# Kernel tuning notes

Measured on AMD Instinct MI355X. Metric: run time of the kernel, lower is better.

## Reference

```python
import jax, jax.numpy as jnp
import numpy as np

COMMITMENT_COST = 0.25


def setup_inputs() -> dict:
    key = jax.random.key(0)
    k1, k2 = jax.random.split(key)
    N, K, D = 65536, 8192, 64
    z_e = jax.random.normal(k1, (N, D), dtype=jnp.float32)
    # xavier_uniform for Embedding(K, D): limit = sqrt(6/(K+D))
    limit = float(np.sqrt(6.0 / (K + D)))
    codebook = jax.random.uniform(k2, (K, D), dtype=jnp.float32, minval=-limit, maxval=limit)
    return {"z_e": z_e, "codebook": codebook}


def reference(z_e, codebook):
    # Squared Euclidean distances; argmin over d^2 == argmin over cdist(p=2)
    x2 = jnp.sum(z_e * z_e, axis=-1, keepdims=True)            # [N,1]
    e2 = jnp.sum(codebook * codebook, axis=-1)                 # [K]
    d2 = x2 - 2.0 * (z_e @ codebook.T) + e2                    # [N,K]
    encoding_indices = jnp.argmin(d2, axis=-1)                 # [N] int

    z_q = codebook[encoding_indices]                           # [N,D] gather

    sg = jax.lax.stop_gradient
    codebook_loss = jnp.mean((z_q - sg(z_e)) ** 2)
    commitment_loss = jnp.mean((z_e - sg(z_q)) ** 2)
    vq_loss = codebook_loss + COMMITMENT_COST * commitment_loss

    # straight-through estimator
    z_q_st = z_e + sg(z_q - z_e)
    return z_q_st, vq_loss, encoding_indices
```

## Files before the change

### kernel.cpp

```cpp
#include <hip/hip_runtime.h>
#include <hip/hip_bf16.h>

#define N_PTS 65536
#define K_CB  8192
#define D_DIM 64
#define CAPS  63

typedef float f32x4 __attribute__((ext_vector_type(4)));
typedef short s16x8 __attribute__((ext_vector_type(8)));

typedef __attribute__((address_space(1))) const unsigned int gu32;
typedef __attribute__((address_space(3))) unsigned int lu32;

__device__ __forceinline__ unsigned bfpack2(float a, float b) {
    union { __hip_bfloat162 h2; unsigned u; } cv;
    cv.h2 = __float22bfloat162_rn(make_float2(a, b));
    return cv.u;
}

__device__ __forceinline__ void gl2lds16(const void* g, void* lds) {
    __builtin_amdgcn_global_load_lds((gu32*)g, (lu32*)lds, 16, 0, 0);
}

template <int CTRL>
__device__ __forceinline__ float dpp_fmax(float v) {
    int s = __builtin_amdgcn_update_dpp(0, __float_as_int(v), CTRL, 0xf, 0xf, true);
    return fmaxf(v, __int_as_float(s));
}

__global__ __launch_bounds__(256) void vq_pack(
        const float* __restrict__ cb, unsigned short* __restrict__ cbswz) {
    int g = blockIdx.x * 256 + threadIdx.x;
    int row = g >> 3, s = g & 7;
    int u = (s ^ (row & 7)) * 8;
    const float4* p = (const float4*)(cb + (size_t)row * D_DIM + u);
    float4 a = p[0], b = p[1];
    uint4 pk;
    pk.x = bfpack2(a.x, a.y); pk.y = bfpack2(a.z, a.w);
    pk.z = bfpack2(b.x, b.y); pk.w = bfpack2(b.z, b.w);
    *(uint4*)(cbswz + (size_t)row * 64 + s * 8) = pk;
}

__global__ __launch_bounds__(256) void vq_prep(
        const float* __restrict__ z, const float* __restrict__ cb,
        float* __restrict__ e2, float* __restrict__ e2n,
        float* __restrict__ x2, float* __restrict__ bmax) {
#pragma clang fp contract(off)
    __shared__ float sm[4];
    int b = blockIdx.x;
    int lane = threadIdx.x & 63;
    int wv = threadIdx.x >> 6;
    const float* src; float* dst; int row0; bool iscb;
    if (b < 128) { src = cb; dst = e2; row0 = b * 64 + wv * 16; iscb = true; }
    else         { src = z;  dst = x2; row0 = (b - 128) * 64 + wv * 16; iscb = false; }
    float lmax = 0.f;
    for (int r = 0; r < 16; ++r) {
        int row = row0 + r;
        float v = src[(size_t)row * D_DIM + lane];
        float w = v * v;
        float ra = w;
#pragma unroll
        for (int i = 1; i < 8; ++i) ra = ra + __shfl(w, lane + 8 * i, 64);
        float r0 = __shfl(ra, 0, 64), r1 = __shfl(ra, 1, 64),
              r2 = __shfl(ra, 2, 64), r3 = __shfl(ra, 3, 64),
              r4 = __shfl(ra, 4, 64), r5 = __shfl(ra, 5, 64),
              r6 = __shfl(ra, 6, 64), r7 = __shfl(ra, 7, 64);
        if (lane == 0) {
            float s = ((r0 + r1) + (r2 + r3)) + ((r4 + r5) + (r6 + r7));
            dst[row] = s;
            if (iscb) e2n[row] = -0.5f * s;
            lmax = fmaxf(lmax, s);
        }
    }
    if (b < 128) {
        if (lane == 0) sm[wv] = lmax;
        __syncthreads();
        if (threadIdx.x == 0)
            bmax[b] = fmaxf(fmaxf(sm[0], sm[1]), fmaxf(sm[2], sm[3]));
    }
}

__device__ __forceinline__ void stage_chunk(
        const unsigned short* __restrict__ cbswz, const float* __restrict__ e2n,
        unsigned short* bufb, float* e2hb, int kc, int w, int l) {
    const char* gbase = (const char*)(cbswz + (size_t)kc * 256 * 64);
#pragma unroll
    for (int j = 0; j < 4; ++j) {
        int off = j * 8192 + w * 1024;
        gl2lds16(gbase + off + l * 16, (char*)bufb + off);
    }
    if (w == 0)
        gl2lds16(e2n + kc * 256 + l * 4, e2hb);
}

__global__ __launch_bounds__(512, 4) void vq_coarse(
        const float* __restrict__ z, const unsigned short* __restrict__ cbswz,
        const float* __restrict__ e2n, const float* __restrict__ x2,
        const float* __restrict__ bmax, int* __restrict__ cand) {
    __shared__ __align__(16) unsigned short pool[4][128 * 64];
    __shared__ __align__(16) float e2h[2][256];
    __shared__ int cntS[128];
    const int tid = threadIdx.x;
    const int w = tid >> 6, l = tid & 63, tx = l & 15, q = l >> 4;
    const int n0 = blockIdx.x * 128;

    if (tid < 128) cntS[tid] = 0;

#pragma unroll
    for (int i = 0; i < 2; ++i) {
        int lin = tid + 512 * i;
        int row = lin >> 3, u = lin & 7;
        const float4* p = (const float4*)(z + (size_t)(n0 + row) * D_DIM + u * 8);
        float4 a = p[0], b2 = p[1];
        uint4 pk;
        pk.x = bfpack2(a.x, a.y);   pk.y = bfpack2(a.z, a.w);
        pk.z = bfpack2(b2.x, b2.y); pk.w = bfpack2(b2.z, b2.w);
        *(uint4*)&pool[0][row * 64 + ((u ^ (row & 7)) * 8)] = pk;
    }

    float e2m;
    {
        float v = fmaxf(bmax[l], bmax[l + 64]);
#pragma unroll
        for (int m = 1; m < 64; m <<= 1) v = fmaxf(v, __shfl_xor(v, m, 64));
        e2m = v;
    }

    float halfW[4], A[4], M[4];
#pragma unroll
    for (int i = 0; i < 4; ++i) {
        int row = n0 + w * 16 + q * 4 + i;
        halfW[i] = 0.0175f * sqrtf(x2[row] * e2m) + 1e-4f;
        A[i] = 3.0e38f;
        M[i] = -3.4e38f;
    }
    float Amin = 3.0e38f;

    __syncthreads();
    s16x8 afr[2];
#pragma unroll
    for (int ks = 0; ks < 2; ++ks) {
        int row = w * 16 + tx;
        afr[ks] = *(const s16x8*)&pool[0][row * 64 + (((ks * 4 + q) ^ (tx & 7)) * 8)];
    }
    __syncthreads();

    stage_chunk(cbswz, e2n, &pool[0][0], e2h[0], 0, w, l);
    __syncthreads();

    for (int it = 0; it < 33; ++it) {
        const int kc = (it < 32) ? it : 0;
        const int cur = it & 1;
        if (it < 32)
            stage_chunk(cbswz, e2n, &pool[((it + 1) & 1) * 2][0], e2h[(it + 1) & 1],
                        (it + 1 < 32) ? it + 1 : 0, w, l);

        const unsigned short* cbb = &pool[cur * 2][0];
        const float* e2c = e2h[cur];
#pragma unroll
        for (int ct = 0; ct < 16; ++ct) {
            int crow = ct * 16 + tx;
            float bias = e2c[crow];
            s16x8 b0 = *(const s16x8*)&cbb[crow * 64 + ((q ^ (tx & 7)) * 8)];
            s16x8 b1 = *(const s16x8*)&cbb[crow * 64 + (((4 + q) ^ (tx & 7)) * 8)];
            f32x4 acc = {bias, bias, bias, bias};
            acc = __builtin_amdgcn_mfma_f32_16x16x32_bf16(afr[0], b0, acc, 0, 0, 0);
            acc = __builtin_amdgcn_mfma_f32_16x16x32_bf16(afr[1], b1, acc, 0, 0, 0);
            M[0] = fmaxf(M[0], acc[0]);
            M[1] = fmaxf(M[1], acc[1]);
            M[2] = fmaxf(M[2], acc[2]);
            M[3] = fmaxf(M[3], acc[3]);
            float amax = fmaxf(fmaxf(fmaxf(acc[0], acc[1]), acc[2]), acc[3]);
            if (amax >= Amin) {
                int kglob = kc * 256 + crow;
#pragma unroll
                for (int r = 0; r < 4; ++r) {
                    if (acc[r] >= A[r]) {
                        int row = w * 16 + q * 4 + r;
                        int slot = atomicAdd(&cntS[row], 1);
                        if (slot < CAPS)
                            cand[(size_t)(n0 + row) * 64 + slot] = kglob;
                    }
                }
            }
        }
        if (it < 32 && ((it == 0) || (it & 1))) {
#pragma unroll
            for (int i = 0; i < 4; ++i) {
                float v = M[i];
                v = dpp_fmax<0xB1>(v);
                v = dpp_fmax<0x4E>(v);
                v = dpp_fmax<0x124>(v);
                v = dpp_fmax<0x128>(v);
                M[i] = v;
                A[i] = v - halfW[i];
            }
            Amin = fminf(fminf(A[0], A[1]), fminf(A[2], A[3]));
        }
        __syncthreads();
    }
    if (tid < 128) cand[(size_t)(n0 + tid) * 64 + 63] = cntS[tid];
}

__device__ __forceinline__ float exact_score(const float* zr, const float* __restrict__ cb,
                                             const float* __restrict__ e2, float x2v, int k) {
    const float4* c4 = (const float4*)(cb + (size_t)k * D_DIM);
    float g = 0.f;
#pragma unroll
    for (int j = 0; j < 16; ++j) {
        float4 v = c4[j];
        g = fmaf(zr[4 * j + 0], v.x, g);
        g = fmaf(zr[4 * j + 1], v.y, g);
        g = fmaf(zr[4 * j + 2], v.z, g);
        g = fmaf(zr[4 * j + 3], v.w, g);
    }
    return fmaf(-2.f, g, x2v) + e2[k];
}

__global__ __launch_bounds__(1024, 4) void vq_rescore(
        const float* __restrict__ z, const float* __restrict__ cb,
        const float* __restrict__ e2, const float* __restrict__ x2,
        int* __restrict__ slots, float* __restrict__ idx_out,
        float* __restrict__ partials) {
    int tid = threadIdx.x;
    int r = tid >> 2, sub = tid & 3;
    int n = blockIdx.x * 256 + r;
    float zr[64];
    const float4* z4 = (const float4*)(z + (size_t)n * D_DIM);
#pragma unroll
    for (int i = 0; i < 16; ++i) {
        float4 v = z4[i];
        zr[4 * i] = v.x; zr[4 * i + 1] = v.y; zr[4 * i + 2] = v.z; zr[4 * i + 3] = v.w;
    }
    float x2v = x2[n];
    int cnt = slots[(size_t)n * 64 + 63];
    float bs = 3.4e38f; int bk = 0x7fffffff;
    if (cnt <= CAPS) {
        for (int i = sub; i < cnt; i += 4) {
            int k = slots[(size_t)n * 64 + i];
            float s = exact_score(zr, cb, e2, x2v, k);
            if (s < bs || (s == bs && k < bk)) { bs = s; bk = k; }
        }
    }
    unsigned long long mask = __ballot(cnt > CAPS && sub == 0);
    while (mask) {
        int src = __ffsll((long long)mask) - 1;
        mask &= (mask - 1);
        int rown = __shfl(n, src, 64);
        float x2s = __shfl(x2v, src, 64);
        float zs[64];
        const float4* zz = (const float4*)(z + (size_t)rown * D_DIM);
#pragma unroll
        for (int i = 0; i < 16; ++i) {
            float4 v = zz[i];
            zs[4 * i] = v.x; zs[4 * i + 1] = v.y; zs[4 * i + 2] = v.z; zs[4 * i + 3] = v.w;
        }
        float fb = 3.4e38f; int fk = 0x7fffffff;
        for (int k = (tid & 63); k < K_CB; k += 64) {
            float s = exact_score(zs, cb, e2, x2s, k);
            if (s < fb || (s == fb && k < fk)) { fb = s; fk = k; }
        }
#pragma unroll
        for (int m = 1; m < 64; m <<= 1) {
            float ov = __shfl_xor(fb, m, 64);
            int   ok = __shfl_xor(fk, m, 64);
            if (ov < fb || (ov == fb && ok < fk)) { fb = ov; fk = ok; }
        }
        if ((tid & 63) == src) { bs = fb; bk = fk; }
    }
#pragma unroll
    for (int m = 1; m < 4; m <<= 1) {
        float ov = __shfl_xor(bs, m, 64);
        int   ok = __shfl_xor(bk, m, 64);
        if (ov < bs || (ov == bs && ok < bk)) { bs = ov; bk = ok; }
    }
    __threadfence_block();

    __shared__ float red[256];
    if (sub == 0) {
        idx_out[n] = (float)bk;
        float lsum = 0.f;
        const float4* c4 = (const float4*)(cb + (size_t)bk * D_DIM);
        float4* o4 = (float4*)((float*)slots + (size_t)n * 64);
#pragma unroll
        for (int j = 0; j < 16; ++j) {
            float4 c = c4[j];
            float4 o;
            float d0 = c.x - zr[4 * j];     o.x = zr[4 * j]     + d0;
            float d1 = c.y - zr[4 * j + 1]; o.y = zr[4 * j + 1] + d1;
            float d2 = c.z - zr[4 * j + 2]; o.z = zr[4 * j + 2] + d2;
            float d3 = c.w - zr[4 * j + 3]; o.w = zr[4 * j + 3] + d3;
            lsum += d0 * d0 + d1 * d1 + d2 * d2 + d3 * d3;
            o4[j] = o;
        }
        red[r] = lsum;
    }
    __syncthreads();
    for (int s = 128; s > 0; s >>= 1) {
        if (tid < s) red[tid] += red[tid + s];
        __syncthreads();
    }
    if (tid == 0) partials[blockIdx.x] = red[0];
}

__global__ void vq_final(const float* __restrict__ partials, float* __restrict__ loss_out) {
    __shared__ float red[256];
    int tid = threadIdx.x;
    red[tid] = partials[tid];
    __syncthreads();
    for (int s = 128; s > 0; s >>= 1) {
        if (tid < s) red[tid] += red[tid + s];
        __syncthreads();
    }
    if (tid == 0) *loss_out = 1.25f * red[0] / (float)(N_PTS * D_DIM);
}

extern "C" void kernel_launch(void* const* d_in, const int* in_sizes, int n_in,
                              void* d_out, int out_size, void* d_ws, size_t ws_size,
                              hipStream_t stream) {
    const float* z  = (const float*)d_in[0];
    const float* cb = (const float*)d_in[1];
    float* out      = (float*)d_out;
    float* zq_out   = out;
    float* loss_out = out + (size_t)N_PTS * D_DIM;
    float* idx_out  = loss_out + 1;

    float* wsf = (float*)d_ws;
    float* partials = wsf;
    float* e2  = wsf + 256;
    float* e2n = wsf + 256 + K_CB;
    float* x2  = wsf + 256 + 2 * K_CB;
    unsigned short* cbswz = (unsigned short*)(wsf + 256 + 2 * K_CB + N_PTS);

    int* cand = (int*)zq_out;
    float* bmax = idx_out;

    vq_pack   <<<K_CB * 8 / 256, 256, 0, stream>>>(cb, cbswz);
    vq_prep   <<<128 + N_PTS / 64, 256, 0, stream>>>(z, cb, e2, e2n, x2, bmax);
    vq_coarse <<<N_PTS / 128, 512, 0, stream>>>(z, cbswz, e2n, x2, bmax, cand);
    vq_rescore<<<N_PTS / 256, 1024, 0, stream>>>(z, cb, e2, x2, cand, idx_out, partials);
    vq_final  <<<1, 256, 0, stream>>>(partials, loss_out);
}
```

Before: 326.8 us.

## Give each coarse wave two row tiles and split codebook columns across wave pairs

In the coarse kernel, each wave now computes two 16-row tiles against half of each 256-entry codebook chunk, so every B fragment loaded from LDS feeds two MFMA chains. A pair of waves merges row maxima through a small shared buffer after each chunk, and thresholds are now refreshed every chunk instead of every other chunk. The rescore kernel drops from four threads per row to two and uses a smaller block. The intent is to cut LDS reads per MFMA and tighten pruning, at the cost of more registers, an extra LDS exchange each iteration, and less parallelism during rescoring.

```diff
diff --git a/kernel.cpp b/kernel.cpp
--- a/kernel.cpp
+++ b/kernel.cpp
@@ -99,9 +99,11 @@
         const float* __restrict__ bmax, int* __restrict__ cand) {
     __shared__ __align__(16) unsigned short pool[4][128 * 64];
     __shared__ __align__(16) float e2h[2][256];
+    __shared__ __align__(16) float mrg[2][2][4][4][8];
     __shared__ int cntS[128];
     const int tid = threadIdx.x;
     const int w = tid >> 6, l = tid & 63, tx = l & 15, q = l >> 4;
+    const int pr = w >> 1, half = w & 1;
     const int n0 = blockIdx.x * 128;
 
     if (tid < 128) cntS[tid] = 0;
@@ -126,10 +128,10 @@
         e2m = v;
     }
 
-    float halfW[4], A[4], M[4];
-#pragma unroll
-    for (int i = 0; i < 4; ++i) {
-        int row = n0 + w * 16 + q * 4 + i;
+    float halfW[8], A[8], M[8];
+#pragma unroll
+    for (int i = 0; i < 8; ++i) {
+        int row = n0 + pr * 32 + (i >> 2) * 16 + q * 4 + (i & 3);
         halfW[i] = 0.0175f * sqrtf(x2[row] * e2m) + 1e-4f;
         A[i] = 3.0e38f;
         M[i] = -3.4e38f;
@@ -137,12 +139,14 @@
     float Amin = 3.0e38f;
 
     __syncthreads();
-    s16x8 afr[2];
-#pragma unroll
-    for (int ks = 0; ks < 2; ++ks) {
-        int row = w * 16 + tx;
-        afr[ks] = *(const s16x8*)&pool[0][row * 64 + (((ks * 4 + q) ^ (tx & 7)) * 8)];
-    }
+    s16x8 afr[2][2];
+#pragma unroll
+    for (int rt = 0; rt < 2; ++rt)
+#pragma unroll
+        for (int ks = 0; ks < 2; ++ks) {
+            int row = pr * 32 + rt * 16 + tx;
+            afr[rt][ks] = *(const s16x8*)&pool[0][row * 64 + (((ks * 4 + q) ^ (tx & 7)) * 8)];
+        }
     __syncthreads();
 
     stage_chunk(cbswz, e2n, &pool[0][0], e2h[0], 0, w, l);
@@ -158,25 +162,44 @@
         const unsigned short* cbb = &pool[cur * 2][0];
         const float* e2c = e2h[cur];
 #pragma unroll
-        for (int ct = 0; ct < 16; ++ct) {
+        for (int c8 = 0; c8 < 8; ++c8) {
+            int ct = half * 8 + c8;
             int crow = ct * 16 + tx;
             float bias = e2c[crow];
             s16x8 b0 = *(const s16x8*)&cbb[crow * 64 + ((q ^ (tx & 7)) * 8)];
             s16x8 b1 = *(const s16x8*)&cbb[crow * 64 + (((4 + q) ^ (tx & 7)) * 8)];
-            f32x4 acc = {bias, bias, bias, bias};
-            acc = __builtin_amdgcn_mfma_f32_16x16x32_bf16(afr[0], b0, acc, 0, 0, 0);
-            acc = __builtin_amdgcn_mfma_f32_16x16x32_bf16(afr[1], b1, acc, 0, 0, 0);
-            M[0] = fmaxf(M[0], acc[0]);
-            M[1] = fmaxf(M[1], acc[1]);
-            M[2] = fmaxf(M[2], acc[2]);
-            M[3] = fmaxf(M[3], acc[3]);
-            float amax = fmaxf(fmaxf(fmaxf(acc[0], acc[1]), acc[2]), acc[3]);
+            f32x4 acc0 = {bias, bias, bias, bias};
+            acc0 = __builtin_amdgcn_mfma_f32_16x16x32_bf16(afr[0][0], b0, acc0, 0, 0, 0);
+            acc0 = __builtin_amdgcn_mfma_f32_16x16x32_bf16(afr[0][1], b1, acc0, 0, 0, 0);
+            f32x4 acc1 = {bias, bias, bias, bias};
+            acc1 = __builtin_amdgcn_mfma_f32_16x16x32_bf16(afr[1][0], b0, acc1, 0, 0, 0);
+            acc1 = __builtin_amdgcn_mfma_f32_16x16x32_bf16(afr[1][1], b1, acc1, 0, 0, 0);
+            M[0] = fmaxf(M[0], acc0[0]);
+            M[1] = fmaxf(M[1], acc0[1]);
+            M[2] = fmaxf(M[2], acc0[2]);
+            M[3] = fmaxf(M[3], acc0[3]);
+            M[4] = fmaxf(M[4], acc1[0]);
+            M[5] = fmaxf(M[5], acc1[1]);
+            M[6] = fmaxf(M[6], acc1[2]);
+            M[7] = fmaxf(M[7], acc1[3]);
+            float amax = fmaxf(
+                fmaxf(fmaxf(acc0[0], acc0[1]), fmaxf(acc0[2], acc0[3])),
+                fmaxf(fmaxf(acc1[0], acc1[1]), fmaxf(acc1[2], acc1[3])));
             if (amax >= Amin) {
                 int kglob = kc * 256 + crow;
 #pragma unroll
                 for (int r = 0; r < 4; ++r) {
-                    if (acc[r] >= A[r]) {
-                        int row = w * 16 + q * 4 + r;
+                    if (acc0[r] >= A[r]) {
+                        int row = pr * 32 + q * 4 + r;
+                        int slot = atomicAdd(&cntS[row], 1);
+                        if (slot < CAPS)
+                            cand[(size_t)(n0 + row) * 64 + slot] = kglob;
+                    }
+                }
+#pragma unroll
+                for (int r = 0; r < 4; ++r) {
+                    if (acc1[r] >= A[4 + r]) {
+                        int row = pr * 32 + 16 + q * 4 + r;
                         int slot = atomicAdd(&cntS[row], 1);
                         if (slot < CAPS)
                             cand[(size_t)(n0 + row) * 64 + slot] = kglob;
@@ -184,20 +207,34 @@
                 }
             }
         }
-        if (it < 32 && ((it == 0) || (it & 1))) {
-#pragma unroll
-            for (int i = 0; i < 4; ++i) {
+        if (it < 32) {
+#pragma unroll
+            for (int i = 0; i < 8; ++i) {
                 float v = M[i];
                 v = dpp_fmax<0xB1>(v);
                 v = dpp_fmax<0x4E>(v);
                 v = dpp_fmax<0x124>(v);
                 v = dpp_fmax<0x128>(v);
                 M[i] = v;
-                A[i] = v - halfW[i];
             }
-            Amin = fminf(fminf(A[0], A[1]), fminf(A[2], A[3]));
+            if (tx == 0) {
+                *(float4*)&mrg[it & 1][half][pr][q][0] = make_float4(M[0], M[1], M[2], M[3]);
+                *(float4*)&mrg[it & 1][half][pr][q][4] = make_float4(M[4], M[5], M[6], M[7]);
+            }
         }
         __syncthreads();
+        if (it < 32) {
+            float4 oa = *(const float4*)&mrg[it & 1][half ^ 1][pr][q][0];
+            float4 ob = *(const float4*)&mrg[it & 1][half ^ 1][pr][q][4];
+            M[0] = fmaxf(M[0], oa.x); M[1] = fmaxf(M[1], oa.y);
+            M[2] = fmaxf(M[2], oa.z); M[3] = fmaxf(M[3], oa.w);
+            M[4] = fmaxf(M[4], ob.x); M[5] = fmaxf(M[5], ob.y);
+            M[6] = fmaxf(M[6], ob.z); M[7] = fmaxf(M[7], ob.w);
+#pragma unroll
+            for (int i = 0; i < 8; ++i) A[i] = M[i] - halfW[i];
+            Amin = fminf(fminf(fminf(A[0], A[1]), fminf(A[2], A[3])),
+                         fminf(fminf(A[4], A[5]), fminf(A[6], A[7])));
+        }
     }
     if (tid < 128) cand[(size_t)(n0 + tid) * 64 + 63] = cntS[tid];
 }
@@ -217,13 +254,13 @@
     return fmaf(-2.f, g, x2v) + e2[k];
 }
 
-__global__ __launch_bounds__(1024, 4) void vq_rescore(
+__global__ __launch_bounds__(512, 2) void vq_rescore(
         const float* __restrict__ z, const float* __restrict__ cb,
         const float* __restrict__ e2, const float* __restrict__ x2,
         int* __restrict__ slots, float* __restrict__ idx_out,
         float* __restrict__ partials) {
     int tid = threadIdx.x;
-    int r = tid >> 2, sub = tid & 3;
+    int r = tid >> 1, half = tid & 1;
     int n = blockIdx.x * 256 + r;
     float zr[64];
     const float4* z4 = (const float4*)(z + (size_t)n * D_DIM);
@@ -236,13 +273,13 @@
     int cnt = slots[(size_t)n * 64 + 63];
     float bs = 3.4e38f; int bk = 0x7fffffff;
     if (cnt <= CAPS) {
-        for (int i = sub; i < cnt; i += 4) {
+        for (int i = half; i < cnt; i += 2) {
             int k = slots[(size_t)n * 64 + i];
             float s = exact_score(zr, cb, e2, x2v, k);
             if (s < bs || (s == bs && k < bk)) { bs = s; bk = k; }
         }
     }
-    unsigned long long mask = __ballot(cnt > CAPS && sub == 0);
+    unsigned long long mask = __ballot(cnt > CAPS && half == 0);
     while (mask) {
         int src = __ffsll((long long)mask) - 1;
         mask &= (mask - 1);
@@ -268,16 +305,15 @@
         }
         if ((tid & 63) == src) { bs = fb; bk = fk; }
     }
-#pragma unroll
-    for (int m = 1; m < 4; m <<= 1) {
-        float ov = __shfl_xor(bs, m, 64);
-        int   ok = __shfl_xor(bk, m, 64);
+    {
+        float ov = __shfl_xor(bs, 1, 64);
+        int   ok = __shfl_xor(bk, 1, 64);
         if (ov < bs || (ov == bs && ok < bk)) { bs = ov; bk = ok; }
     }
     __threadfence_block();
 
     __shared__ float red[256];
-    if (sub == 0) {
+    if (half == 0) {
         idx_out[n] = (float)bk;
         float lsum = 0.f;
         const float4* c4 = (const float4*)(cb + (size_t)bk * D_DIM);
@@ -338,6 +374,6 @@
     vq_pack   <<<K_CB * 8 / 256, 256, 0, stream>>>(cb, cbswz);
     vq_prep   <<<128 + N_PTS / 64, 256, 0, stream>>>(z, cb, e2, e2n, x2, bmax);
     vq_coarse <<<N_PTS / 128, 512, 0, stream>>>(z, cbswz, e2n, x2, bmax, cand);
-    vq_rescore<<<N_PTS / 256, 1024, 0, stream>>>(z, cb, e2, x2, cand, idx_out, partials);
+    vq_rescore<<<N_PTS / 256, 512, 0, stream>>>(z, cb, e2, x2, cand, idx_out, partials);
     vq_final  <<<1, 256, 0, stream>>>(partials, loss_out);
 }
```

Measured after the change: 380.1 us. 1.16x slower.

## Split coarse codebook scan across two blocks per point tile with global candidate counters

Applied to the files above, without the earlier changes.

The coarse pass now launches twice as many blocks, each scanning half of the codebook for the same 128 points. Per-block LDS drops to half, so launch bounds allow 8 waves per SIMD and occupancy can rise. Candidate counters move from shared memory to global atomics on the cand buffer, zeroed in vq_pack. The rescore kernel uses 2 threads per point instead of 4. The risks are more global atomic traffic, a looser pruning threshold because each half only sees its own maxima, and more candidate overflows that fall back to the full scan.

```diff
diff --git a/kernel.cpp b/kernel.cpp
--- a/kernel.cpp
+++ b/kernel.cpp
@@ -29,7 +29,8 @@
 }
 
 __global__ __launch_bounds__(256) void vq_pack(
-        const float* __restrict__ cb, unsigned short* __restrict__ cbswz) {
+        const float* __restrict__ cb, unsigned short* __restrict__ cbswz,
+        int* __restrict__ cand) {
     int g = blockIdx.x * 256 + threadIdx.x;
     int row = g >> 3, s = g & 7;
     int u = (s ^ (row & 7)) * 8;
@@ -39,6 +40,7 @@
     pk.x = bfpack2(a.x, a.y); pk.y = bfpack2(a.z, a.w);
     pk.z = bfpack2(b.x, b.y); pk.w = bfpack2(b.z, b.w);
     *(uint4*)(cbswz + (size_t)row * 64 + s * 8) = pk;
+    cand[(size_t)g * 64 + 63] = 0;
 }
 
 __global__ __launch_bounds__(256) void vq_prep(
@@ -81,30 +83,30 @@
 }
 
 __device__ __forceinline__ void stage_chunk(
-        const unsigned short* __restrict__ cbswz, const float* __restrict__ e2n,
+        const unsigned short* __restrict__ cbS, const float* __restrict__ e2S,
         unsigned short* bufb, float* e2hb, int kc, int w, int l) {
-    const char* gbase = (const char*)(cbswz + (size_t)kc * 256 * 64);
-#pragma unroll
-    for (int j = 0; j < 4; ++j) {
+    const char* gbase = (const char*)(cbS + (size_t)kc * 128 * 64);
+#pragma unroll
+    for (int j = 0; j < 2; ++j) {
         int off = j * 8192 + w * 1024;
         gl2lds16(gbase + off + l * 16, (char*)bufb + off);
     }
-    if (w == 0)
-        gl2lds16(e2n + kc * 256 + l * 4, e2hb);
-}
-
-__global__ __launch_bounds__(512, 4) void vq_coarse(
+    if (w == 0 && l < 32)
+        gl2lds16(e2S + kc * 128 + l * 4, e2hb);
+}
+
+__global__ __launch_bounds__(512, 8) void vq_coarse(
         const float* __restrict__ z, const unsigned short* __restrict__ cbswz,
         const float* __restrict__ e2n, const float* __restrict__ x2,
         const float* __restrict__ bmax, int* __restrict__ cand) {
-    __shared__ __align__(16) unsigned short pool[4][128 * 64];
-    __shared__ __align__(16) float e2h[2][256];
-    __shared__ int cntS[128];
+    __shared__ __align__(16) unsigned short pool[2][128 * 64];
+    __shared__ __align__(16) float e2h[2][128];
     const int tid = threadIdx.x;
     const int w = tid >> 6, l = tid & 63, tx = l & 15, q = l >> 4;
-    const int n0 = blockIdx.x * 128;
-
-    if (tid < 128) cntS[tid] = 0;
+    const int n0 = (blockIdx.x >> 1) * 128;
+    const int koff = (blockIdx.x & 1) * (K_CB / 2);
+    const unsigned short* cbS = cbswz + (size_t)koff * 64;
+    const float* e2S = e2n + koff;
 
 #pragma unroll
     for (int i = 0; i < 2; ++i) {
@@ -145,20 +147,21 @@
     }
     __syncthreads();
 
-    stage_chunk(cbswz, e2n, &pool[0][0], e2h[0], 0, w, l);
-    __syncthreads();
-
-    for (int it = 0; it < 33; ++it) {
-        const int kc = (it < 32) ? it : 0;
+    stage_chunk(cbS, e2S, pool[0], e2h[0], 0, w, l);
+    __syncthreads();
+
+    for (int it = 0; it < 34; ++it) {
+        const int kc = (it < 32) ? it : it - 32;
         const int cur = it & 1;
-        if (it < 32)
-            stage_chunk(cbswz, e2n, &pool[((it + 1) & 1) * 2][0], e2h[(it + 1) & 1],
-                        (it + 1 < 32) ? it + 1 : 0, w, l);
-
-        const unsigned short* cbb = &pool[cur * 2][0];
+        if (it < 33) {
+            int nk = (it + 1 < 32) ? it + 1 : it - 31;
+            stage_chunk(cbS, e2S, pool[cur ^ 1], e2h[cur ^ 1], nk, w, l);
+        }
+
+        const unsigned short* cbb = pool[cur];
         const float* e2c = e2h[cur];
 #pragma unroll
-        for (int ct = 0; ct < 16; ++ct) {
+        for (int ct = 0; ct < 8; ++ct) {
             int crow = ct * 16 + tx;
             float bias = e2c[crow];
             s16x8 b0 = *(const s16x8*)&cbb[crow * 64 + ((q ^ (tx & 7)) * 8)];
@@ -170,21 +173,21 @@
             M[1] = fmaxf(M[1], acc[1]);
             M[2] = fmaxf(M[2], acc[2]);
             M[3] = fmaxf(M[3], acc[3]);
-            float amax = fmaxf(fmaxf(fmaxf(acc[0], acc[1]), acc[2]), acc[3]);
+            float amax = fmaxf(fmaxf(acc[0], acc[1]), fmaxf(acc[2], acc[3]));
             if (amax >= Amin) {
-                int kglob = kc * 256 + crow;
+                int kglob = koff + kc * 128 + crow;
 #pragma unroll
                 for (int r = 0; r < 4; ++r) {
                     if (acc[r] >= A[r]) {
-                        int row = w * 16 + q * 4 + r;
-                        int slot = atomicAdd(&cntS[row], 1);
+                        int row = n0 + w * 16 + q * 4 + r;
+                        int slot = atomicAdd(&cand[(size_t)row * 64 + 63], 1);
                         if (slot < CAPS)
-                            cand[(size_t)(n0 + row) * 64 + slot] = kglob;
+                            cand[(size_t)row * 64 + slot] = kglob;
                     }
                 }
             }
         }
-        if (it < 32 && ((it == 0) || (it & 1))) {
+        if (it >= 1 && it < 32) {
 #pragma unroll
             for (int i = 0; i < 4; ++i) {
                 float v = M[i];
@@ -199,7 +202,6 @@
         }
         __syncthreads();
     }
-    if (tid < 128) cand[(size_t)(n0 + tid) * 64 + 63] = cntS[tid];
 }
 
 __device__ __forceinline__ float exact_score(const float* zr, const float* __restrict__ cb,
@@ -217,13 +219,13 @@
     return fmaf(-2.f, g, x2v) + e2[k];
 }
 
-__global__ __launch_bounds__(1024, 4) void vq_rescore(
+__global__ __launch_bounds__(512, 2) void vq_rescore(
         const float* __restrict__ z, const float* __restrict__ cb,
         const float* __restrict__ e2, const float* __restrict__ x2,
         int* __restrict__ slots, float* __restrict__ idx_out,
         float* __restrict__ partials) {
     int tid = threadIdx.x;
-    int r = tid >> 2, sub = tid & 3;
+    int r = tid >> 1, half = tid & 1;
     int n = blockIdx.x * 256 + r;
     float zr[64];
     const float4* z4 = (const float4*)(z + (size_t)n * D_DIM);
@@ -236,13 +238,13 @@
     int cnt = slots[(size_t)n * 64 + 63];
     float bs = 3.4e38f; int bk = 0x7fffffff;
     if (cnt <= CAPS) {
-        for (int i = sub; i < cnt; i += 4) {
+        for (int i = half; i < cnt; i += 2) {
             int k = slots[(size_t)n * 64 + i];
             float s = exact_score(zr, cb, e2, x2v, k);
             if (s < bs || (s == bs && k < bk)) { bs = s; bk = k; }
         }
     }
-    unsigned long long mask = __ballot(cnt > CAPS && sub == 0);
+    unsigned long long mask = __ballot(cnt > CAPS && half == 0);
     while (mask) {
         int src = __ffsll((long long)mask) - 1;
         mask &= (mask - 1);
@@ -268,16 +270,15 @@
         }
         if ((tid & 63) == src) { bs = fb; bk = fk; }
     }
-#pragma unroll
-    for (int m = 1; m < 4; m <<= 1) {
-        float ov = __shfl_xor(bs, m, 64);
-        int   ok = __shfl_xor(bk, m, 64);
+    {
+        float ov = __shfl_xor(bs, 1, 64);
+        int   ok = __shfl_xor(bk, 1, 64);
         if (ov < bs || (ov == bs && ok < bk)) { bs = ov; bk = ok; }
     }
     __threadfence_block();
 
     __shared__ float red[256];
-    if (sub == 0) {
+    if (half == 0) {
         idx_out[n] = (float)bk;
         float lsum = 0.f;
         const float4* c4 = (const float4*)(cb + (size_t)bk * D_DIM);
@@ -335,9 +336,9 @@
     int* cand = (int*)zq_out;
     float* bmax = idx_out;
 
-    vq_pack   <<<K_CB * 8 / 256, 256, 0, stream>>>(cb, cbswz);
+    vq_pack   <<<K_CB * 8 / 256, 256, 0, stream>>>(cb, cbswz, cand);
     vq_prep   <<<128 + N_PTS / 64, 256, 0, stream>>>(z, cb, e2, e2n, x2, bmax);
-    vq_coarse <<<N_PTS / 128, 512, 0, stream>>>(z, cbswz, e2n, x2, bmax, cand);
-    vq_rescore<<<N_PTS / 256, 1024, 0, stream>>>(z, cb, e2, x2, cand, idx_out, partials);
+    vq_coarse <<<2 * (N_PTS / 128), 512, 0, stream>>>(z, cbswz, e2n, x2, bmax, cand);
+    vq_rescore<<<N_PTS / 256, 512, 0, stream>>>(z, cb, e2, x2, cand, idx_out, partials);
     vq_final  <<<1, 256, 0, stream>>>(partials, loss_out);
 }
```

Result: slower. 542.7 us (+66.0%).
